# Kernel optimization log

Measured on AMD Instinct MI355X. Metric: run time of the kernel, lower is better.

## Reference

```python
import jax, jax.numpy as jnp
import numpy as np
from jax import lax

# Module hyperparameters (init_kwargs)
B, T, F, H = 512, 256, 64, 128
D = F + H            # decoder LSTMCell width = input_dim + hidden_rnn
OUT_DIM = 32         # output_dim (survival horizon steps)
RISKS = 2
NEG = -1e10


def lstm_cell(x, h, c, Wih, Whh):
    # PyTorch gate order: i, f, g, o; bias=False
    g = x @ Wih.T + h @ Whh.T
    i, f, gg, o = jnp.split(g, 4, axis=-1)
    c = jax.nn.sigmoid(f) * c + jax.nn.sigmoid(i) * jnp.tanh(gg)
    h = jax.nn.sigmoid(o) * jnp.tanh(c)
    return h, c


def setup_inputs() -> dict:
    key = jax.random.key(0)
    ks = jax.random.split(key, 12)
    rn = lambda k, shp, fan: jax.random.normal(k, shp, jnp.float32) * (1.0 / np.sqrt(fan))
    return {
        "x": jax.random.normal(ks[0], (B, T, F), jnp.float32),
        # encoder LSTM (1 layer, bias=False)
        "W_ih_emb": rn(ks[1], (4 * H, F), F),
        "W_hh_emb": rn(ks[2], (4 * H, H), H),
        # longitudinal head: Linear(H -> F)
        "W_long": rn(ks[3], (F, H), H),
        "b_long": jnp.zeros((F,), jnp.float32),
        # attention head: Linear(F+H -> 1)
        "W_att": rn(ks[4], (1, D), D),
        "b_att": jnp.zeros((1,), jnp.float32),
        # per-risk cause-specific LSTMCell (bias=False) and Linear(D -> 1)
        "W_ih_cs": rn(ks[5], (RISKS, 4 * D, D), D),
        "W_hh_cs": rn(ks[6], (RISKS, 4 * D, D), D),
        "W_cs": rn(ks[7], (RISKS, 1, D), D),
        "b_cs": jnp.zeros((RISKS, 1), jnp.float32),
    }


def _forward(x, W_ih_emb, W_hh_emb, W_long, b_long, W_att, b_att,
             W_ih_cs, W_hh_cs, W_cs, b_cs):
    inputmask = jnp.abs(x).sum(2) == 0                      # [B,T]
    last_obs = (~inputmask).sum(axis=1) - 1                 # [B]

    # encoder LSTM over time
    def enc_step(carry, xt):
        h, c = carry
        h, c = lstm_cell(xt, h, c, W_ih_emb, W_hh_emb)
        return (h, c), h

    h0 = jnp.zeros((x.shape[0], H), x.dtype)
    _, hs = lax.scan(enc_step, (h0, h0), x.transpose(1, 0, 2))
    hidden = hs.transpose(1, 0, 2)                          # [B,T,H]

    long_pred = hidden @ W_long.T + b_long                  # [B,T,F]

    x_last = x[jnp.arange(x.shape[0]), last_obs]            # [B,F]
    concat = jnp.concatenate(
        [hidden, jnp.broadcast_to(x_last[:, None, :], (x.shape[0], x.shape[1], F))], -1)
    scores = (concat @ W_att.T + b_att)[..., 0]             # [B,T]

    idx = jnp.arange(x.shape[1])[None, :]
    scores = jnp.where(idx >= last_obs[:, None], NEG, scores)
    att = jax.nn.softmax(scores, axis=1)
    att = jnp.where((last_obs > 0)[:, None], att, 0.0)      # rows with last_obs==0 zeroed

    hidden_att = jnp.einsum('bt,bth->bh', att, hidden)      # [B,H]
    ha = jnp.concatenate([hidden_att, x_last], 1)           # [B,D]

    state0 = (lax.stop_gradient(ha), lax.stop_gradient(ha))  # .detach() on init state
    rs = jnp.arange(OUT_DIM * RISKS) % RISKS                # k-major, r-minor loop order

    def dec_step(carry, r):
        h, c = carry
        h, c = lstm_cell(ha, h, c, W_ih_cs[r], W_hh_cs[r])
        out = jax.nn.sigmoid(h @ W_cs[r].T + b_cs[r])       # [B,1]
        return (h, c), out

    _, outs = lax.scan(dec_step, state0, rs)                # [steps,B,1]
    outcomes = jax.nn.softmax(outs[..., 0].T, axis=-1)      # [B, OUT_DIM*RISKS]
    parts = tuple(outcomes[:, i * OUT_DIM:(i + 1) * OUT_DIM] for i in range(RISKS))
    return (long_pred,) + parts


def reference(x, W_ih_emb, W_hh_emb, W_long, b_long, W_att, b_att,
              W_ih_cs, W_hh_cs, W_cs, b_cs):
    return _forward(x, W_ih_emb, W_hh_emb, W_long, b_long, W_att, b_att,
                    W_ih_cs, W_hh_cs, W_cs, b_cs)
```

## Files before the change

### kernel.cpp

```cpp
#include <hip/hip_runtime.h>
#include <stdint.h>

#define DEV __device__ __forceinline__
typedef unsigned short u16; typedef unsigned int u32; typedef unsigned long long u64;
typedef __attribute__((ext_vector_type(8))) short s8v;
typedef __attribute__((ext_vector_type(4))) float f4v;

#define Bb 512
#define Tt 256
#define Ff 64
#define Hh 128
#define Dd 192
#define L2E  1.4426950408889634f
#define L2E2 2.8853900817779268f

DEV u16 f2bf(float f){ u32 u = __builtin_bit_cast(u32, f); u32 r = (u + 0x7fffu + ((u>>16)&1u)) >> 16; return (u16)r; }
DEV float sigm(float x){ return __builtin_amdgcn_rcpf(1.0f + __expf(-x)); }
DEV float ex2(float x){ float r; asm("v_exp_f32 %0, %1" : "=v"(r) : "v"(x)); return r; }
DEV float sig2n(float y){ return __builtin_amdgcn_rcpf(1.0f + ex2(y)); }
DEV float th2 (float y){ return 1.0f - 2.0f*__builtin_amdgcn_rcpf(1.0f + ex2(y)); }
DEV u32 cvtpk(float lo, float hi){ u32 d; asm("v_cvt_pk_bf16_f32 %0, %1, %2" : "=v"(d) : "v"(lo), "v"(hi)); return d; }
DEV float blo(u32 q){ return __builtin_bit_cast(float, q<<16); }
DEV float bhi(u32 q){ return __builtin_bit_cast(float, q & 0xffff0000u); }

DEV f4v mfma16(s8v a, s8v b, f4v c){ return __builtin_amdgcn_mfma_f32_16x16x32_bf16(a, b, c, 0, 0, 0); }
DEV void barrier_lds(){ asm volatile("s_waitcnt lgkmcnt(0)\n\ts_barrier" ::: "memory"); }

DEV void dma16(const void* g, void* l){
  __builtin_amdgcn_global_load_lds((const __attribute__((address_space(1))) void*)g,
                                   (__attribute__((address_space(3))) void*)l, 16, 0, 0);
}

DEV int hxe2(int k, int c){ return (k>>5)*512 + (((k>>3)&3)*16 + c)*8 + (k&7); }

DEV s8v pack8s(const float* p, float sc){
  const float4 a = *(const float4*)p; const float4 b = *(const float4*)(p+4);
  s8v r; r[0]=(short)f2bf(a.x*sc); r[1]=(short)f2bf(a.y*sc); r[2]=(short)f2bf(a.z*sc); r[3]=(short)f2bf(a.w*sc);
  r[4]=(short)f2bf(b.x*sc); r[5]=(short)f2bf(b.y*sc); r[6]=(short)f2bf(b.z*sc); r[7]=(short)f2bf(b.w*sc); return r;
}
DEV s8v pack8(const float* p){ return pack8s(p, 1.0f); }
DEV u32 pk2(float a, float b){ return (u32)f2bf(a) | ((u32)f2bf(b)<<16); }

__global__ __launch_bounds__(64) void prelim_k(const float* __restrict__ x,
    const float* __restrict__ Watt, const float* __restrict__ batt,
    float* __restrict__ xlast, float* __restrict__ c0, int* __restrict__ lastobs)
{
  int b = blockIdx.x, tid = threadIdx.x;
  int cnt = 0;
  for (int it = 0; it < 4; ++it){
    int t = it*64 + tid;
    const float4* p = (const float4*)(x + ((size_t)b*Tt + t)*Ff);
    float s = 0.0f;
    #pragma unroll
    for (int q = 0; q < 16; ++q){ float4 v = p[q]; s += fabsf(v.x)+fabsf(v.y)+fabsf(v.z)+fabsf(v.w); }
    u64 m = __ballot(s != 0.0f);
    cnt += __popcll(m);
  }
  int last = cnt - 1;
  int li = (last < 0) ? (Tt-1) : last;
  float xl = x[((size_t)b*Tt + li)*Ff + tid];
  xlast[b*Ff + tid] = xl;
  float p = xl * Watt[Hh + tid];
  for (int off = 32; off; off >>= 1) p += __shfl_down(p, off);
  if (tid == 0){ c0[b] = (p + batt[0]) * L2E; lastobs[b] = last; }
}

__global__ __launch_bounds__(256) void prep_wd_k(const float* __restrict__ Whhcs,
    const float* __restrict__ Wihcs, u16* __restrict__ Wd, u16* __restrict__ WdIH)
{
  int idx = blockIdx.x*256 + threadIdx.x;
  int j = idx & 7, lane = (idx>>3)&63;
  int f = idx>>9;
  int kt = f % 6; int mtr = f/6;
  int mt = mtr % 48, r = mtr/48;
  int ut = mt>>2, g = mt&3;
  int row = g*Dd + ut*16 + (lane&15);
  int k = kt*32 + (lane>>4)*8 + j;
  float sc = (g == 2) ? L2E2 : -L2E;
  size_t src = ((size_t)r*768 + row)*Dd + k;
  Wd[idx]   = f2bf(Whhcs[src] * sc);
  WdIH[idx] = f2bf(Wihcs[src] * sc);
}

__global__ __launch_bounds__(64) void xw_k(const u16* __restrict__ WdIH,
    const float* __restrict__ ha, u16* __restrict__ xwg)
{
  int lane = threadIdx.x, l15 = lane&15, l4 = lane>>4;
  int cg = blockIdx.x & 3, rm = blockIdx.x >> 2;
  s8v af[6];
  #pragma unroll
  for (int kt=0;kt<6;++kt) af[kt] = *(const s8v*)(WdIH + (size_t)(rm*6+kt)*512 + lane*8);
  #pragma unroll
  for (int ct=0; ct<8; ++ct){
    int c = cg*128 + ct*16 + l15;
    f4v a = {0,0,0,0};
    #pragma unroll
    for (int kt=0;kt<6;++kt){
      s8v b = pack8(ha + (size_t)c*Dd + kt*32 + l4*8);
      a = mfma16(af[kt], b, a);
    }
    int bg = cg*8 + ct;
    int base = bg*24576 + rm*256 + l15*16 + l4*4;
    *(u32*)&xwg[base]   = pk2(a[0], a[1]);
    *(u32*)&xwg[base+2] = pk2(a[2], a[3]);
  }
}

__global__ __launch_bounds__(512)
__attribute__((amdgpu_waves_per_eu(2,2)))
void enc_k(
    const float* __restrict__ x, const float* __restrict__ Whh, const float* __restrict__ Wih,
    const float* __restrict__ Wlong, const float* __restrict__ blong, const float* __restrict__ Watt,
    const float* __restrict__ xlast, const float* __restrict__ c0v, const int* __restrict__ lastobs,
    float* __restrict__ lp_out, float* __restrict__ ha)
{
  __shared__ __align__(16) u16 hx[2][3072];
  __shared__ float sarr[2][16];
  const int tid = threadIdx.x, wid = tid>>6, lane = tid&63, l15 = lane&15, l4 = lane>>4;
  const int b0 = blockIdx.x*16;
  const int xrow = tid>>5, xc2 = (tid&31)*2;

  s8v wf[4][6];
  #pragma unroll
  for (int mt = 0; mt < 4; ++mt){
    int gate = mt*Hh + wid*16 + l15;
    float sc = (mt == 2) ? L2E2 : -L2E;
    #pragma unroll
    for (int kt = 0; kt < 6; ++kt){
      int k0 = kt*32 + l4*8;
      if (kt < 4) wf[mt][kt] = pack8s(Whh + (size_t)gate*Hh + k0, sc);
      else        wf[mt][kt] = pack8s(Wih + (size_t)gate*Ff + (k0 - Hh), sc);
    }
  }
  s8v wfx[6];
  {
    s8v z = {0,0,0,0,0,0,0,0};
    #pragma unroll
    for (int kt = 0; kt < 6; ++kt) wfx[kt] = z;
    if (wid < 4){
      int f = wid*16 + l15;
      #pragma unroll
      for (int kt = 0; kt < 4; ++kt) wfx[kt] = pack8(Wlong + (size_t)f*Hh + kt*32 + l4*8);
    } else if (wid == 4 && l15 == 0){
      #pragma unroll
      for (int kt = 0; kt < 4; ++kt) wfx[kt] = pack8s(Watt + kt*32 + l4*8, L2E);
    }
  }
  float bl[4] = {0,0,0,0};
  if (wid < 4){
    #pragma unroll
    for (int j = 0; j < 4; ++j) bl[j] = blong[wid*16 + l4*4 + j];
  }
  const int   lastb = lastobs[b0 + l15];
  const float c0b   = c0v[b0 + l15];

  const int he0 = hxe2(wid*16 + l4*4, l15);
  const int xe0 = hxe2(Hh + xc2, xrow);
  float* lpb = lp_out + ((size_t)(b0+l15)*Tt)*Ff + wid*16 + l4*4;

  ((u64*)hx[0])[tid] = 0ull;
  {
    float2 xv = *(const float2*)(x + ((size_t)(b0+xrow)*Tt + 0)*Ff + xc2);
    *(u32*)&hx[0][xe0] = cvtpk(xv.x, xv.y);
  }
  float2 xa = *(const float2*)(x + ((size_t)(b0+xrow)*Tt + 1)*Ff + xc2);
  float2 xb;
  __syncthreads();

  float cst[4] = {0,0,0,0}, hp[4] = {0,0,0,0}, hpp[4] = {0,0,0,0};
  float accA[4] = {0,0,0,0}, mrun = -3.0e38f, zrun = 0.0f;

#define ENC_STEP(T_, CURB_, NXTB_, XC_, XN_) { \
    const int t = (T_); \
    s8v bf[6]; \
    _Pragma("unroll") \
    for (int kt = 0; kt < 6; ++kt) \
      bf[kt] = *(const s8v*)&hx[CURB_][kt*512 + lane*8]; \
    { int tp = t + 2; if (tp > Tt-1) tp = Tt-1; \
      XN_ = *(const float2*)(x + ((size_t)(b0+xrow)*Tt + tp)*Ff + xc2); } \
    f4v acc0 = {0,0,0,0}, acc1 = {0,0,0,0}, acc2 = {0,0,0,0}, acc3 = {0,0,0,0}, accx = {0,0,0,0}; \
    _Pragma("unroll") \
    for (int kt = 0; kt < 6; ++kt){ \
      acc0 = mfma16(wf[0][kt], bf[kt], acc0); \
      acc1 = mfma16(wf[1][kt], bf[kt], acc1); \
      acc2 = mfma16(wf[2][kt], bf[kt], acc2); \
      acc3 = mfma16(wf[3][kt], bf[kt], acc3); \
    } \
    if (wid < 5){ \
      _Pragma("unroll") \
      for (int kt = 0; kt < 6; ++kt) accx = mfma16(wfx[kt], bf[kt], accx); \
    } \
    if (wid == 4 && l4 == 0) sarr[NXTB_][l15] = accx[0] + c0b; \
    float hnew[4]; \
    _Pragma("unroll") \
    for (int j = 0; j < 4; ++j){ \
      float si = sig2n(acc0[j]), sf = sig2n(acc1[j]); \
      float tg = th2(acc2[j]),   so = sig2n(acc3[j]); \
      float cn = sf*cst[j] + si*tg; \
      cst[j] = cn; \
      hnew[j] = so * th2(cn * L2E2); \
    } \
    if (t >= 2){ \
      float sv = sarr[CURB_][l15]; \
      if (t-2 < lastb){ \
        float mn = fmaxf(mrun, sv); \
        float sc = ex2(mrun - mn); \
        float e  = ex2(sv - mn); \
        zrun = zrun*sc + e; \
        _Pragma("unroll") \
        for (int j = 0; j < 4; ++j) accA[j] = accA[j]*sc + e*hpp[j]; \
        mrun = mn; \
      } \
    } \
    _Pragma("unroll") \
    for (int j = 0; j < 4; ++j){ hpp[j] = hp[j]; hp[j] = hnew[j]; } \
    { u32 plo = cvtpk(hnew[0], hnew[1]), phi = cvtpk(hnew[2], hnew[3]); \
      *(u64*)&hx[NXTB_][he0] = (u64)plo | ((u64)phi<<32); } \
    if (t < Tt-1) *(u32*)&hx[NXTB_][xe0] = cvtpk(XC_.x, XC_.y); \
    if (wid < 4 && t >= 1){ \
      float4 v; v.x = accx[0]+bl[0]; v.y = accx[1]+bl[1]; v.z = accx[2]+bl[2]; v.w = accx[3]+bl[3]; \
      *(float4*)(lpb + (size_t)(t-1)*Ff) = v; \
    } \
    barrier_lds(); }

  for (int tp2 = 0; tp2 < 128; ++tp2){
    ENC_STEP(2*tp2,   0, 1, xa, xb)
    ENC_STEP(2*tp2+1, 1, 0, xb, xa)
  }
#undef ENC_STEP

  {
    if (254 < lastb){
      float sv = sarr[0][l15];
      float mn = fmaxf(mrun, sv);
      float sc = ex2(mrun - mn);
      float e  = ex2(sv - mn);
      zrun = zrun*sc + e;
      #pragma unroll
      for (int j = 0; j < 4; ++j) accA[j] = accA[j]*sc + e*hpp[j];
      mrun = mn;
    }
    s8v bfE[4];
    #pragma unroll
    for (int kt = 0; kt < 4; ++kt)
      bfE[kt] = *(const s8v*)&hx[0][kt*512 + lane*8];
    if (wid < 4){
      f4v accx = {0,0,0,0};
      #pragma unroll
      for (int kt = 0; kt < 4; ++kt) accx = mfma16(wfx[kt], bfE[kt], accx);
      float4 v; v.x = accx[0]+bl[0]; v.y = accx[1]+bl[1]; v.z = accx[2]+bl[2]; v.w = accx[3]+bl[3];
      *(float4*)(lpb + (size_t)(Tt-1)*Ff) = v;
    }
    float inv = (zrun > 0.0f) ? __builtin_amdgcn_rcpf(zrun) : 0.0f;
    #pragma unroll
    for (int j = 0; j < 4; ++j)
      ha[(size_t)(b0 + l15)*Dd + wid*16 + l4*4 + j] = accA[j]*inv;
    __syncthreads();
    for (int q = tid; q < 16*Ff; q += 512){
      int r2 = q >> 6, f = q & 63;
      ha[(size_t)(b0 + r2)*Dd + Hh + f] = xlast[(b0 + r2)*Ff + f];
    }
  }
}

__global__ __launch_bounds__(768, 3)
void dec_k(const float* __restrict__ ha, const u16* __restrict__ Wd,
    const u16* __restrict__ xwg, const float* __restrict__ Wcs,
    const float* __restrict__ bcs, float* __restrict__ outs)
{
  __shared__ __align__(16) u16 hx[2][3072];
  __shared__ __align__(16) u16 wstr[12*12*512];
  __shared__ float red[2][12][16];
  const int tid = threadIdx.x, wid = tid>>6, lane = tid&63, l15 = lane&15, l4 = lane>>4;
  const int b0 = blockIdx.x*16;

  {
    int k = (tid>>4)*4, c = tid&15;
    float4 v = *(const float4*)(ha + (size_t)(b0+c)*Dd + k);
    int e = hxe2(k, c);
    *(u32*)&hx[0][e]   = cvtpk(v.x, v.y);
    *(u32*)&hx[0][e+2] = cvtpk(v.z, v.w);
  }
  u32 xwr[2][4][2];
  #pragma unroll
  for (int r = 0; r < 2; ++r)
    #pragma unroll
    for (int g = 0; g < 4; ++g){
      int base = blockIdx.x*24576 + (r*48 + wid*4 + g)*256 + l15*16 + l4*4;
      u64 q = *(const u64*)&xwg[base];
      xwr[r][g][0] = (u32)q; xwr[r][g][1] = (u32)(q>>32);
    }
  const int u0 = wid*16 + l4*4;
  float cst[4], wcs0[4], wcs1[4];
  #pragma unroll
  for (int j = 0; j < 4; ++j){
    cst[j]  = ha[(size_t)(b0+l15)*Dd + u0 + j];
    wcs0[j] = Wcs[u0 + j];
    wcs1[j] = Wcs[Dd + u0 + j];
  }
  const float bc0 = bcs[0], bc1 = bcs[1];
  const int he0 = hxe2(u0, l15);
  u16* const wring = &wstr[wid*12*512];
  __syncthreads();

#define WSRC(R_, KT_, G_) (Wd + (size_t)(((R_)*48 + wid*4 + (G_))*6 + (KT_))*512 + lane*8)
#define ISSUE_G(RT_, KTT_, KTG_) { \
    dma16(WSRC(RT_, KTT_, 0), wring + ((4*(KTG_)+0)%12)*512); \
    dma16(WSRC(RT_, KTT_, 1), wring + ((4*(KTG_)+1)%12)*512); \
    dma16(WSRC(RT_, KTT_, 2), wring + ((4*(KTG_)+2)%12)*512); \
    dma16(WSRC(RT_, KTT_, 3), wring + ((4*(KTG_)+3)%12)*512); }
#define GRP(CURB_, KTG_) { \
    asm volatile("s_waitcnt vmcnt(8)" ::: "memory"); \
    s8v q0 = *(const s8v*)(wring + ((4*(KTG_)+0)%12)*512 + lane*8); \
    s8v q1 = *(const s8v*)(wring + ((4*(KTG_)+1)%12)*512 + lane*8); \
    s8v q2 = *(const s8v*)(wring + ((4*(KTG_)+2)%12)*512 + lane*8); \
    s8v q3 = *(const s8v*)(wring + ((4*(KTG_)+3)%12)*512 + lane*8); \
    s8v bf = *(const s8v*)&hx[CURB_][(KTG_)*512 + lane*8]; \
    a0 = mfma16(q0, bf, a0); a1 = mfma16(q1, bf, a1); \
    a2 = mfma16(q2, bf, a2); a3 = mfma16(q3, bf, a3); }

#define XWI(R_) { \
    u32 lo, hi; \
    lo = xwr[R_][0][0]; hi = xwr[R_][0][1]; a0[0]=blo(lo); a0[1]=bhi(lo); a0[2]=blo(hi); a0[3]=bhi(hi); \
    lo = xwr[R_][1][0]; hi = xwr[R_][1][1]; a1[0]=blo(lo); a1[1]=bhi(lo); a1[2]=blo(hi); a1[3]=bhi(hi); \
    lo = xwr[R_][2][0]; hi = xwr[R_][2][1]; a2[0]=blo(lo); a2[1]=bhi(lo); a2[2]=blo(hi); a2[3]=bhi(hi); \
    lo = xwr[R_][3][0]; hi = xwr[R_][3][1]; a3[0]=blo(lo); a3[1]=bhi(lo); a3[2]=blo(hi); a3[3]=bhi(hi); }

#define CELLS(WCS_, NXTB_, PAR_, BC_, S_) { \
    float part = 0.0f, hn[4]; \
    _Pragma("unroll") for (int j = 0; j < 4; ++j){ \
      float si = sig2n(a0[j]), sf = sig2n(a1[j]); \
      float tg = th2(a2[j]),   so = sig2n(a3[j]); \
      float cn = sf*cst[j] + si*tg; \
      cst[j] = cn; \
      hn[j] = so * th2(cn * L2E2); \
      part += hn[j] * WCS_[j]; } \
    { u32 plo = cvtpk(hn[0], hn[1]), phi = cvtpk(hn[2], hn[3]); \
      *(u64*)&hx[NXTB_][he0] = (u64)plo | ((u64)phi<<32); } \
    part += __shfl_xor(part, 16); part += __shfl_xor(part, 32); \
    if (l4 == 0) red[PAR_][wid][l15] = part; \
    barrier_lds(); \
    if (tid < 16){ \
      float ss = BC_; \
      _Pragma("unroll") for (int q = 0; q < 12; ++q) ss += red[PAR_][q][tid]; \
      outs[(S_)*Bb + b0 + tid] = sigm(ss); } }

#define DEC_STEP(R_, RN_, CURB_, NXTB_, WCS_, BC_, PAR_, S_) { \
    f4v a0, a1, a2, a3; \
    XWI(R_) \
    GRP(CURB_, 0) ISSUE_G(R_,  3, 0) \
    GRP(CURB_, 1) ISSUE_G(R_,  4, 1) \
    GRP(CURB_, 2) ISSUE_G(R_,  5, 2) \
    GRP(CURB_, 3) ISSUE_G(RN_, 0, 3) \
    GRP(CURB_, 4) ISSUE_G(RN_, 1, 4) \
    GRP(CURB_, 5) ISSUE_G(RN_, 2, 5) \
    CELLS(WCS_, NXTB_, PAR_, BC_, S_) }

  ISSUE_G(0, 0, 0); ISSUE_G(0, 1, 1); ISSUE_G(0, 2, 2);

  for (int sp = 0; sp < 32; ++sp){
    DEC_STEP(0, 1, 0, 1, wcs0, bc0, 0, sp*2)
    DEC_STEP(1, 0, 1, 0, wcs1, bc1, 1, sp*2+1)
  }
  asm volatile("s_waitcnt vmcnt(0)" ::: "memory");
#undef WSRC
#undef ISSUE_G
#undef GRP
#undef XWI
#undef CELLS
#undef DEC_STEP
}

__global__ __launch_bounds__(256) void fin_k(const float* __restrict__ outs, float* __restrict__ dout)
{
  int row = blockIdx.x*256 + threadIdx.x;
  float v[64]; float mx = -3.0e38f;
  #pragma unroll
  for (int s = 0; s < 64; ++s){ v[s] = outs[s*Bb + row]; mx = fmaxf(mx, v[s]); }
  float sum = 0.0f;
  #pragma unroll
  for (int s = 0; s < 64; ++s){ v[s] = __expf(v[s] - mx); sum += v[s]; }
  float inv = __builtin_amdgcn_rcpf(sum);
  float* p0 = dout + (size_t)Bb*Tt*Ff;
  float* p1 = p0 + Bb*32;
  #pragma unroll
  for (int j = 0; j < 32; ++j) p0[row*32 + j] = v[j]*inv;
  #pragma unroll
  for (int j = 0; j < 32; ++j) p1[row*32 + j] = v[32 + j]*inv;
}

extern "C" void kernel_launch(void* const* d_in, const int* in_sizes, int n_in,
                              void* d_out, int out_size, void* d_ws, size_t ws_size,
                              hipStream_t stream)
{
  const float* x      = (const float*)d_in[0];
  const float* Wih    = (const float*)d_in[1];
  const float* Whh    = (const float*)d_in[2];
  const float* Wlong  = (const float*)d_in[3];
  const float* blong  = (const float*)d_in[4];
  const float* Watt   = (const float*)d_in[5];
  const float* batt   = (const float*)d_in[6];
  const float* Wihcs  = (const float*)d_in[7];
  const float* Whhcs  = (const float*)d_in[8];
  const float* Wcs    = (const float*)d_in[9];
  const float* bcs    = (const float*)d_in[10];
  float* out = (float*)d_out;
  char* ws = (char*)d_ws;

  float* xlast   = (float*)ws;
  float* c0      = (float*)(ws + 131072);
  int*   lastobs = (int*)  (ws + 133120);
  float* ha      = (float*)(ws + 135168);
  u16*   Wd      = (u16*)  (ws + 528384);
  u16*   WdIH    = (u16*)  (ws + 1118208);
  u16*   xwg     = (u16*)  (ws + 1708032);
  float* outs    = (float*)(ws + 3280896);

  prep_wd_k<<<1152, 256, 0, stream>>>(Whhcs, Wihcs, Wd, WdIH);
  prelim_k<<<Bb, 64, 0, stream>>>(x, Watt, batt, xlast, c0, lastobs);
  enc_k<<<32, 512, 0, stream>>>(x, Whh, Wih, Wlong, blong, Watt, xlast, c0, lastobs, out, ha);
  xw_k<<<384, 64, 0, stream>>>(WdIH, ha, xwg);
  dec_k<<<32, 768, 0, stream>>>(ha, Wd, xwg, Wcs, bcs, outs);
  fin_k<<<2, 256, 0, stream>>>(outs, out);
}
```

Measured before the change: 546.8 us.

## Process two 16-row batch tiles per encoder block and fuse LSTM gate math

The encoder kernel now handles 32 batch rows per block as two independent 16-row streams, interleaving their MFMA chains and gate math between the same barriers. The grid drops from 32 to 16 blocks. The goal is to hide the latency of the serial recurrence by giving each wave two independent dependency chains, and to halve the number of per-step barriers across the device. The gate nonlinearities are also rewritten with shared reciprocals, cutting rcp instructions per element. The risks are higher register pressure, more work per step on each CU, and half as many CUs in use.

```diff
diff --git a/kernel.cpp b/kernel.cpp
--- a/kernel.cpp
+++ b/kernel.cpp
@@ -114,10 +114,10 @@
     const float* __restrict__ xlast, const float* __restrict__ c0v, const int* __restrict__ lastobs,
     float* __restrict__ lp_out, float* __restrict__ ha)
 {
-  __shared__ __align__(16) u16 hx[2][3072];
-  __shared__ float sarr[2][16];
+  __shared__ __align__(16) u16 hx[2][2][3072];
+  __shared__ float sarr[2][2][16];
   const int tid = threadIdx.x, wid = tid>>6, lane = tid&63, l15 = lane&15, l4 = lane>>4;
-  const int b0 = blockIdx.x*16;
+  const int b0 = blockIdx.x*32;
   const int xrow = tid>>5, xc2 = (tid&31)*2;
 
   s8v wf[4][6];
@@ -151,112 +151,153 @@
     #pragma unroll
     for (int j = 0; j < 4; ++j) bl[j] = blong[wid*16 + l4*4 + j];
   }
-  const int   lastb = lastobs[b0 + l15];
-  const float c0b   = c0v[b0 + l15];
+  const int   lastbA = lastobs[b0 + l15],      lastbB = lastobs[b0 + 16 + l15];
+  const float c0bA   = c0v[b0 + l15],          c0bB   = c0v[b0 + 16 + l15];
 
   const int he0 = hxe2(wid*16 + l4*4, l15);
   const int xe0 = hxe2(Hh + xc2, xrow);
-  float* lpb = lp_out + ((size_t)(b0+l15)*Tt)*Ff + wid*16 + l4*4;
-
-  ((u64*)hx[0])[tid] = 0ull;
+  float* lpbA = lp_out + ((size_t)(b0+l15)*Tt)*Ff + wid*16 + l4*4;
+  float* lpbB = lp_out + ((size_t)(b0+16+l15)*Tt)*Ff + wid*16 + l4*4;
+  const float* xA = x + ((size_t)(b0+xrow)*Tt)*Ff + xc2;
+  const float* xB = x + ((size_t)(b0+16+xrow)*Tt)*Ff + xc2;
+
+  ((u64*)&hx[0][0][0])[tid] = 0ull;
+  ((u64*)&hx[1][0][0])[tid] = 0ull;
+  { float2 v = *(const float2*)xA; *(u32*)&hx[0][0][xe0] = cvtpk(v.x, v.y); }
+  { float2 v = *(const float2*)xB; *(u32*)&hx[1][0][xe0] = cvtpk(v.x, v.y); }
+  float2 xaA = *(const float2*)(xA + (size_t)1*Ff);
+  float2 xaB = *(const float2*)(xB + (size_t)1*Ff);
+  float2 xbA, xbB;
+  __syncthreads();
+
+  float cstA[4]={0,0,0,0}, hpA[4]={0,0,0,0}, hppA[4]={0,0,0,0}, attA[4]={0,0,0,0};
+  float cstB[4]={0,0,0,0}, hpB[4]={0,0,0,0}, hppB[4]={0,0,0,0}, attB[4]={0,0,0,0};
+  float mrunA=-3.0e38f, zrunA=0.0f, mrunB=-3.0e38f, zrunB=0.0f;
+
+#define CELL7(A0_, A1_, A2_, A3_, CST_, HN_) { \
+    _Pragma("unroll") for (int j = 0; j < 4; ++j){ \
+      float I_ = ex2(A0_[j]), F_ = ex2(A1_[j]), G_ = ex2(A2_[j]), O_ = ex2(A3_[j]); \
+      float Aq = (1.0f + I_)*(G_ + 1.0f), Bq = 1.0f + F_; \
+      float r1 = __builtin_amdgcn_rcpf(Aq*Bq); \
+      float cn = r1*(CST_[j]*Aq + Bq*(G_ - 1.0f)); \
+      CST_[j] = cn; \
+      float CN_ = ex2(cn * L2E2); \
+      float r2 = __builtin_amdgcn_rcpf((1.0f + O_)*(CN_ + 1.0f)); \
+      HN_[j] = (CN_ - 1.0f)*r2; } }
+
+#define ATT_UPD(SV_, LASTB_, MRUN_, ZRUN_, ATT_, HPP_) { \
+    if (t-2 < LASTB_){ \
+      float mn = fmaxf(MRUN_, SV_); \
+      float sc = ex2(MRUN_ - mn); \
+      float e  = ex2(SV_ - mn); \
+      ZRUN_ = ZRUN_*sc + e; \
+      _Pragma("unroll") for (int j = 0; j < 4; ++j) ATT_[j] = ATT_[j]*sc + e*HPP_[j]; \
+      MRUN_ = mn; } }
+
+#define ENC_STEP(T_, CURB_, NXTB_, XCA_, XNA_, XCB_, XNB_) { \
+    const int t = (T_); \
+     \
+    s8v bfA[6]; \
+    _Pragma("unroll") for (int kt = 0; kt < 6; ++kt) bfA[kt] = *(const s8v*)&hx[0][CURB_][kt*512 + lane*8]; \
+    f4v aA0={0,0,0,0}, aA1={0,0,0,0}, aA2={0,0,0,0}, aA3={0,0,0,0}, axA={0,0,0,0}; \
+    _Pragma("unroll") for (int kt = 0; kt < 6; ++kt){ \
+      aA0 = mfma16(wf[0][kt], bfA[kt], aA0); aA1 = mfma16(wf[1][kt], bfA[kt], aA1); \
+      aA2 = mfma16(wf[2][kt], bfA[kt], aA2); aA3 = mfma16(wf[3][kt], bfA[kt], aA3); } \
+    if (wid < 5){ _Pragma("unroll") for (int kt = 0; kt < 6; ++kt) axA = mfma16(wfx[kt], bfA[kt], axA); } \
+     \
+    s8v bfB[6]; \
+    _Pragma("unroll") for (int kt = 0; kt < 6; ++kt) bfB[kt] = *(const s8v*)&hx[1][CURB_][kt*512 + lane*8]; \
+    f4v aB0={0,0,0,0}, aB1={0,0,0,0}, aB2={0,0,0,0}, aB3={0,0,0,0}, axB={0,0,0,0}; \
+    _Pragma("unroll") for (int kt = 0; kt < 6; ++kt){ \
+      aB0 = mfma16(wf[0][kt], bfB[kt], aB0); aB1 = mfma16(wf[1][kt], bfB[kt], aB1); \
+      aB2 = mfma16(wf[2][kt], bfB[kt], aB2); aB3 = mfma16(wf[3][kt], bfB[kt], aB3); } \
+    if (wid < 5){ _Pragma("unroll") for (int kt = 0; kt < 6; ++kt) axB = mfma16(wfx[kt], bfB[kt], axB); } \
+     \
+    { int tp = t + 2; if (tp > Tt-1) tp = Tt-1; \
+      XNA_ = *(const float2*)(xA + (size_t)tp*Ff); \
+      XNB_ = *(const float2*)(xB + (size_t)tp*Ff); } \
+    if (wid == 4 && l4 == 0){ sarr[0][NXTB_][l15] = axA[0] + c0bA; sarr[1][NXTB_][l15] = axB[0] + c0bB; } \
+    float hnA[4], hnB[4]; \
+    CELL7(aA0, aA1, aA2, aA3, cstA, hnA) \
+    CELL7(aB0, aB1, aB2, aB3, cstB, hnB) \
+    if (t >= 2){ \
+      float svA = sarr[0][CURB_][l15]; \
+      ATT_UPD(svA, lastbA, mrunA, zrunA, attA, hppA) \
+      float svB = sarr[1][CURB_][l15]; \
+      ATT_UPD(svB, lastbB, mrunB, zrunB, attB, hppB) \
+    } \
+    _Pragma("unroll") for (int j = 0; j < 4; ++j){ \
+      hppA[j] = hpA[j]; hpA[j] = hnA[j]; hppB[j] = hpB[j]; hpB[j] = hnB[j]; } \
+    { u32 p0 = cvtpk(hnA[0], hnA[1]), p1 = cvtpk(hnA[2], hnA[3]); \
+      *(u64*)&hx[0][NXTB_][he0] = (u64)p0 | ((u64)p1<<32); } \
+    { u32 p0 = cvtpk(hnB[0], hnB[1]), p1 = cvtpk(hnB[2], hnB[3]); \
+      *(u64*)&hx[1][NXTB_][he0] = (u64)p0 | ((u64)p1<<32); } \
+    if (t < Tt-1){ \
+      *(u32*)&hx[0][NXTB_][xe0] = cvtpk(XCA_.x, XCA_.y); \
+      *(u32*)&hx[1][NXTB_][xe0] = cvtpk(XCB_.x, XCB_.y); } \
+    if (wid < 4 && t >= 1){ \
+      float4 v; v.x = axA[0]+bl[0]; v.y = axA[1]+bl[1]; v.z = axA[2]+bl[2]; v.w = axA[3]+bl[3]; \
+      *(float4*)(lpbA + (size_t)(t-1)*Ff) = v; \
+      float4 w; w.x = axB[0]+bl[0]; w.y = axB[1]+bl[1]; w.z = axB[2]+bl[2]; w.w = axB[3]+bl[3]; \
+      *(float4*)(lpbB + (size_t)(t-1)*Ff) = w; } \
+    barrier_lds(); }
+
+  for (int tp2 = 0; tp2 < 128; ++tp2){
+    ENC_STEP(2*tp2,   0, 1, xaA, xbA, xaB, xbB)
+    ENC_STEP(2*tp2+1, 1, 0, xbA, xaA, xbB, xaB)
+  }
+#undef ENC_STEP
+#undef ATT_UPD
+#undef CELL7
+
   {
-    float2 xv = *(const float2*)(x + ((size_t)(b0+xrow)*Tt + 0)*Ff + xc2);
-    *(u32*)&hx[0][xe0] = cvtpk(xv.x, xv.y);
-  }
-  float2 xa = *(const float2*)(x + ((size_t)(b0+xrow)*Tt + 1)*Ff + xc2);
-  float2 xb;
-  __syncthreads();
-
-  float cst[4] = {0,0,0,0}, hp[4] = {0,0,0,0}, hpp[4] = {0,0,0,0};
-  float accA[4] = {0,0,0,0}, mrun = -3.0e38f, zrun = 0.0f;
-
-#define ENC_STEP(T_, CURB_, NXTB_, XC_, XN_) { \
-    const int t = (T_); \
-    s8v bf[6]; \
-    _Pragma("unroll") \
-    for (int kt = 0; kt < 6; ++kt) \
-      bf[kt] = *(const s8v*)&hx[CURB_][kt*512 + lane*8]; \
-    { int tp = t + 2; if (tp > Tt-1) tp = Tt-1; \
-      XN_ = *(const float2*)(x + ((size_t)(b0+xrow)*Tt + tp)*Ff + xc2); } \
-    f4v acc0 = {0,0,0,0}, acc1 = {0,0,0,0}, acc2 = {0,0,0,0}, acc3 = {0,0,0,0}, accx = {0,0,0,0}; \
-    _Pragma("unroll") \
-    for (int kt = 0; kt < 6; ++kt){ \
-      acc0 = mfma16(wf[0][kt], bf[kt], acc0); \
-      acc1 = mfma16(wf[1][kt], bf[kt], acc1); \
-      acc2 = mfma16(wf[2][kt], bf[kt], acc2); \
-      acc3 = mfma16(wf[3][kt], bf[kt], acc3); \
-    } \
-    if (wid < 5){ \
-      _Pragma("unroll") \
-      for (int kt = 0; kt < 6; ++kt) accx = mfma16(wfx[kt], bf[kt], accx); \
-    } \
-    if (wid == 4 && l4 == 0) sarr[NXTB_][l15] = accx[0] + c0b; \
-    float hnew[4]; \
-    _Pragma("unroll") \
-    for (int j = 0; j < 4; ++j){ \
-      float si = sig2n(acc0[j]), sf = sig2n(acc1[j]); \
-      float tg = th2(acc2[j]),   so = sig2n(acc3[j]); \
-      float cn = sf*cst[j] + si*tg; \
-      cst[j] = cn; \
-      hnew[j] = so * th2(cn * L2E2); \
-    } \
-    if (t >= 2){ \
-      float sv = sarr[CURB_][l15]; \
-      if (t-2 < lastb){ \
-        float mn = fmaxf(mrun, sv); \
-        float sc = ex2(mrun - mn); \
-        float e  = ex2(sv - mn); \
-        zrun = zrun*sc + e; \
-        _Pragma("unroll") \
-        for (int j = 0; j < 4; ++j) accA[j] = accA[j]*sc + e*hpp[j]; \
-        mrun = mn; \
-      } \
-    } \
-    _Pragma("unroll") \
-    for (int j = 0; j < 4; ++j){ hpp[j] = hp[j]; hp[j] = hnew[j]; } \
-    { u32 plo = cvtpk(hnew[0], hnew[1]), phi = cvtpk(hnew[2], hnew[3]); \
-      *(u64*)&hx[NXTB_][he0] = (u64)plo | ((u64)phi<<32); } \
-    if (t < Tt-1) *(u32*)&hx[NXTB_][xe0] = cvtpk(XC_.x, XC_.y); \
-    if (wid < 4 && t >= 1){ \
-      float4 v; v.x = accx[0]+bl[0]; v.y = accx[1]+bl[1]; v.z = accx[2]+bl[2]; v.w = accx[3]+bl[3]; \
-      *(float4*)(lpb + (size_t)(t-1)*Ff) = v; \
-    } \
-    barrier_lds(); }
-
-  for (int tp2 = 0; tp2 < 128; ++tp2){
-    ENC_STEP(2*tp2,   0, 1, xa, xb)
-    ENC_STEP(2*tp2+1, 1, 0, xb, xa)
-  }
-#undef ENC_STEP
-
-  {
-    if (254 < lastb){
-      float sv = sarr[0][l15];
-      float mn = fmaxf(mrun, sv);
-      float sc = ex2(mrun - mn);
+    if (254 < lastbA){
+      float sv = sarr[0][0][l15];
+      float mn = fmaxf(mrunA, sv);
+      float sc = ex2(mrunA - mn);
       float e  = ex2(sv - mn);
-      zrun = zrun*sc + e;
-      #pragma unroll
-      for (int j = 0; j < 4; ++j) accA[j] = accA[j]*sc + e*hpp[j];
-      mrun = mn;
-    }
-    s8v bfE[4];
-    #pragma unroll
-    for (int kt = 0; kt < 4; ++kt)
-      bfE[kt] = *(const s8v*)&hx[0][kt*512 + lane*8];
+      zrunA = zrunA*sc + e;
+      #pragma unroll
+      for (int j = 0; j < 4; ++j) attA[j] = attA[j]*sc + e*hppA[j];
+      mrunA = mn;
+    }
+    if (254 < lastbB){
+      float sv = sarr[1][0][l15];
+      float mn = fmaxf(mrunB, sv);
+      float sc = ex2(mrunB - mn);
+      float e  = ex2(sv - mn);
+      zrunB = zrunB*sc + e;
+      #pragma unroll
+      for (int j = 0; j < 4; ++j) attB[j] = attB[j]*sc + e*hppB[j];
+      mrunB = mn;
+    }
     if (wid < 4){
-      f4v accx = {0,0,0,0};
-      #pragma unroll
-      for (int kt = 0; kt < 4; ++kt) accx = mfma16(wfx[kt], bfE[kt], accx);
-      float4 v; v.x = accx[0]+bl[0]; v.y = accx[1]+bl[1]; v.z = accx[2]+bl[2]; v.w = accx[3]+bl[3];
-      *(float4*)(lpb + (size_t)(Tt-1)*Ff) = v;
-    }
-    float inv = (zrun > 0.0f) ? __builtin_amdgcn_rcpf(zrun) : 0.0f;
-    #pragma unroll
-    for (int j = 0; j < 4; ++j)
-      ha[(size_t)(b0 + l15)*Dd + wid*16 + l4*4 + j] = accA[j]*inv;
+      s8v bfEA[4], bfEB[4];
+      #pragma unroll
+      for (int kt = 0; kt < 4; ++kt){
+        bfEA[kt] = *(const s8v*)&hx[0][0][kt*512 + lane*8];
+        bfEB[kt] = *(const s8v*)&hx[1][0][kt*512 + lane*8];
+      }
+      f4v axA = {0,0,0,0}, axB = {0,0,0,0};
+      #pragma unroll
+      for (int kt = 0; kt < 4; ++kt){
+        axA = mfma16(wfx[kt], bfEA[kt], axA);
+        axB = mfma16(wfx[kt], bfEB[kt], axB);
+      }
+      float4 v; v.x = axA[0]+bl[0]; v.y = axA[1]+bl[1]; v.z = axA[2]+bl[2]; v.w = axA[3]+bl[3];
+      *(float4*)(lpbA + (size_t)(Tt-1)*Ff) = v;
+      float4 w; w.x = axB[0]+bl[0]; w.y = axB[1]+bl[1]; w.z = axB[2]+bl[2]; w.w = axB[3]+bl[3];
+      *(float4*)(lpbB + (size_t)(Tt-1)*Ff) = w;
+    }
+    float invA = (zrunA > 0.0f) ? __builtin_amdgcn_rcpf(zrunA) : 0.0f;
+    float invB = (zrunB > 0.0f) ? __builtin_amdgcn_rcpf(zrunB) : 0.0f;
+    #pragma unroll
+    for (int j = 0; j < 4; ++j){
+      ha[(size_t)(b0 + l15)*Dd + wid*16 + l4*4 + j]      = attA[j]*invA;
+      ha[(size_t)(b0 + 16 + l15)*Dd + wid*16 + l4*4 + j] = attB[j]*invB;
+    }
     __syncthreads();
-    for (int q = tid; q < 16*Ff; q += 512){
+    for (int q = tid; q < 32*Ff; q += 512){
       int r2 = q >> 6, f = q & 63;
       ha[(size_t)(b0 + r2)*Dd + Hh + f] = xlast[(b0 + r2)*Ff + f];
     }
@@ -418,7 +459,7 @@
 
   prep_wd_k<<<1152, 256, 0, stream>>>(Whhcs, Wihcs, Wd, WdIH);
   prelim_k<<<Bb, 64, 0, stream>>>(x, Watt, batt, xlast, c0, lastobs);
-  enc_k<<<32, 512, 0, stream>>>(x, Whh, Wih, Wlong, blong, Watt, xlast, c0, lastobs, out, ha);
+  enc_k<<<16, 512, 0, stream>>>(x, Whh, Wih, Wlong, blong, Watt, xlast, c0, lastobs, out, ha);
   xw_k<<<384, 64, 0, stream>>>(WdIH, ha, xwg);
   dec_k<<<32, 768, 0, stream>>>(ha, Wd, xwg, Wcs, bcs, outs);
   fin_k<<<2, 256, 0, stream>>>(outs, out);
```

Result: slower. 771.0 us (+41.0%).

## Fold decoder weight prep into encoder launch and cut transcendental ops in cell

Applied to the files above, without the earlier changes.

Removes the separate prep_wd_k launch and runs its weight conversion in extra blocks (32 to 607) of the encoder kernel, so the conversion can overlap the latency-bound 32-block encoder instead of running serially before it. The LSTM cell update is also rewritten to share reciprocals: one rcp for the i, f and g gates combined and one for o with tanh(c), in place of six separate rcp calls. The algebraic form multiplies several (1+exp) terms together, which could overflow for large pre-activations. The extra blocks also compete with the encoder for CU resources.

```diff
diff --git a/kernel.cpp b/kernel.cpp
--- a/kernel.cpp
+++ b/kernel.cpp
@@ -41,6 +41,16 @@
 DEV s8v pack8(const float* p){ return pack8s(p, 1.0f); }
 DEV u32 pk2(float a, float b){ return (u32)f2bf(a) | ((u32)f2bf(b)<<16); }
 
+#define CELL7_J(A0_, A1_, A2_, A3_, CSTJ_, HNJ_) { \
+    float I_ = ex2(A0_), F_ = ex2(A1_), G_ = ex2(A2_), O_ = ex2(A3_); \
+    float Aq = (1.0f + I_)*(G_ + 1.0f), Bq = 1.0f + F_; \
+    float r1 = __builtin_amdgcn_rcpf(Aq*Bq); \
+    float cn = r1*((CSTJ_)*Aq + Bq*(G_ - 1.0f)); \
+    CSTJ_ = cn; \
+    float CN_ = ex2(cn * L2E2); \
+    float r2 = __builtin_amdgcn_rcpf((1.0f + O_)*(CN_ + 1.0f)); \
+    HNJ_ = (CN_ - 1.0f)*r2; }
+
 __global__ __launch_bounds__(64) void prelim_k(const float* __restrict__ x,
     const float* __restrict__ Watt, const float* __restrict__ batt,
     float* __restrict__ xlast, float* __restrict__ c0, int* __restrict__ lastobs)
@@ -65,23 +75,6 @@
   if (tid == 0){ c0[b] = (p + batt[0]) * L2E; lastobs[b] = last; }
 }
 
-__global__ __launch_bounds__(256) void prep_wd_k(const float* __restrict__ Whhcs,
-    const float* __restrict__ Wihcs, u16* __restrict__ Wd, u16* __restrict__ WdIH)
-{
-  int idx = blockIdx.x*256 + threadIdx.x;
-  int j = idx & 7, lane = (idx>>3)&63;
-  int f = idx>>9;
-  int kt = f % 6; int mtr = f/6;
-  int mt = mtr % 48, r = mtr/48;
-  int ut = mt>>2, g = mt&3;
-  int row = g*Dd + ut*16 + (lane&15);
-  int k = kt*32 + (lane>>4)*8 + j;
-  float sc = (g == 2) ? L2E2 : -L2E;
-  size_t src = ((size_t)r*768 + row)*Dd + k;
-  Wd[idx]   = f2bf(Whhcs[src] * sc);
-  WdIH[idx] = f2bf(Wihcs[src] * sc);
-}
-
 __global__ __launch_bounds__(64) void xw_k(const u16* __restrict__ WdIH,
     const float* __restrict__ ha, u16* __restrict__ xwg)
 {
@@ -112,8 +105,25 @@
     const float* __restrict__ x, const float* __restrict__ Whh, const float* __restrict__ Wih,
     const float* __restrict__ Wlong, const float* __restrict__ blong, const float* __restrict__ Watt,
     const float* __restrict__ xlast, const float* __restrict__ c0v, const int* __restrict__ lastobs,
-    float* __restrict__ lp_out, float* __restrict__ ha)
-{
+    float* __restrict__ lp_out, float* __restrict__ ha,
+    const float* __restrict__ Whhcs, const float* __restrict__ Wihcs,
+    u16* __restrict__ Wd, u16* __restrict__ WdIH)
+{
+  if (blockIdx.x >= 32){
+    int idx = (blockIdx.x - 32)*512 + threadIdx.x;
+    int j = idx & 7, lane2 = (idx>>3)&63;
+    int f = idx>>9;
+    int kt = f % 6; int mtr = f/6;
+    int mt = mtr % 48, r = mtr/48;
+    int ut = mt>>2, g = mt&3;
+    int row = g*Dd + ut*16 + (lane2&15);
+    int k = kt*32 + (lane2>>4)*8 + j;
+    float sc = (g == 2) ? L2E2 : -L2E;
+    size_t src = ((size_t)r*768 + row)*Dd + k;
+    Wd[idx]   = f2bf(Whhcs[src] * sc);
+    WdIH[idx] = f2bf(Wihcs[src] * sc);
+    return;
+  }
   __shared__ __align__(16) u16 hx[2][3072];
   __shared__ float sarr[2][16];
   const int tid = threadIdx.x, wid = tid>>6, lane = tid&63, l15 = lane&15, l4 = lane>>4;
@@ -194,11 +204,7 @@
     float hnew[4]; \
     _Pragma("unroll") \
     for (int j = 0; j < 4; ++j){ \
-      float si = sig2n(acc0[j]), sf = sig2n(acc1[j]); \
-      float tg = th2(acc2[j]),   so = sig2n(acc3[j]); \
-      float cn = sf*cst[j] + si*tg; \
-      cst[j] = cn; \
-      hnew[j] = so * th2(cn * L2E2); \
+      CELL7_J(acc0[j], acc1[j], acc2[j], acc3[j], cst[j], hnew[j]) \
     } \
     if (t >= 2){ \
       float sv = sarr[CURB_][l15]; \
@@ -416,9 +422,9 @@
   u16*   xwg     = (u16*)  (ws + 1708032);
   float* outs    = (float*)(ws + 3280896);
 
-  prep_wd_k<<<1152, 256, 0, stream>>>(Whhcs, Wihcs, Wd, WdIH);
   prelim_k<<<Bb, 64, 0, stream>>>(x, Watt, batt, xlast, c0, lastobs);
-  enc_k<<<32, 512, 0, stream>>>(x, Whh, Wih, Wlong, blong, Watt, xlast, c0, lastobs, out, ha);
+  enc_k<<<608, 512, 0, stream>>>(x, Whh, Wih, Wlong, blong, Watt, xlast, c0, lastobs, out, ha,
+                                 Whhcs, Wihcs, Wd, WdIH);
   xw_k<<<384, 64, 0, stream>>>(WdIH, ha, xwg);
   dec_k<<<32, 768, 0, stream>>>(ha, Wd, xwg, Wcs, bcs, outs);
   fin_k<<<2, 256, 0, stream>>>(outs, out);
```

After: 532.9 us. 1.03x faster.
